# Performance work log

Measured on AMD Instinct MI355X. Metric: run time of the kernel, lower is better.

Reference implementation:

```python
import jax, jax.numpy as jnp
import numpy as np

UP = 4  # FCUUp up_stride
EPS_FCU = 1e-6
EPS_NL = 1e-5


def setup_inputs() -> dict:
    key = jax.random.key(0)
    ks = jax.random.split(key, 24)
    B, E, C, CI = 8, 768, 256, 128
    H, W = 14, 14
    x_t = jax.random.normal(ks[0], (B, 1 + H * W, E), jnp.float32)
    x_cnn = jax.random.normal(ks[1], (B, C, H * UP, W * UP), jnp.float32)
    s = 0.02
    return {
        'x_t': x_t,
        'x_cnn': x_cnn,
        # FCUUp: conv_project (E->C) + BN
        'Wp': jax.random.normal(ks[2], (C, E), jnp.float32) * s,
        'bp': jnp.zeros((C,), jnp.float32),
        'g1': jnp.ones((C,), jnp.float32),
        'b1': jnp.zeros((C,), jnp.float32),
        'rm1': jax.random.normal(ks[3], (C,), jnp.float32) * 0.1,
        'rv1': jax.random.uniform(ks[4], (C,), jnp.float32, 0.5, 1.5),
        # NLBlockND (embedded): g, theta, phi 1x1 convs C->CI
        'Wg': jax.random.normal(ks[5], (CI, C), jnp.float32) * s,
        'bg': jnp.zeros((CI,), jnp.float32),
        'Wth': jax.random.normal(ks[6], (CI, C), jnp.float32) * s,
        'bth': jnp.zeros((CI,), jnp.float32),
        'Wph': jax.random.normal(ks[7], (CI, C), jnp.float32) * s,
        'bph': jnp.zeros((CI,), jnp.float32),
        # W_z: 1x1 conv CI->C + BN
        'Wz': jax.random.normal(ks[8], (C, CI), jnp.float32) * s,
        'bz': jnp.zeros((C,), jnp.float32),
        'g2': jax.random.normal(ks[9], (C,), jnp.float32) * 0.1,
        'b2': jax.random.normal(ks[10], (C,), jnp.float32) * 0.1,
        'rm2': jax.random.normal(ks[11], (C,), jnp.float32) * 0.1,
        'rv2': jax.random.uniform(ks[12], (C,), jnp.float32, 0.5, 1.5),
    }


def _bn(x, gamma, beta, mean, var, eps):
    # eval-mode BatchNorm2d over channel axis 1 of BCHW
    inv = gamma / jnp.sqrt(var + eps)
    return x * inv[None, :, None, None] + (beta - mean * inv)[None, :, None, None]


def _conv1x1(x, w, b):
    # x: BCHW, w: [O, C] -> BOHW
    return jnp.einsum('oc,bchw->bohw', w, x) + b[None, :, None, None]


def reference(x_t, x_cnn, Wp, bp, g1, b1, rm1, rv1, Wg, bg, Wth, bth, Wph, bph, Wz, bz, g2, b2, rm2, rv2):
    B, Nc, H2, W2 = x_cnn.shape
    H, W = H2 // UP, W2 // UP
    CI = Wg.shape[0]
    # --- FCUUp: tokens -> feature map ---
    xr = x_t[:, 1:].transpose(0, 2, 1).reshape(B, -1, H, W)  # B,E,H,W
    xr = jax.nn.relu(_bn(_conv1x1(xr, Wp, bp), g1, b1, rm1, rv1, EPS_FCU))
    x_up = jnp.repeat(jnp.repeat(xr, UP, axis=2), UP, axis=3)  # nearest interp -> B,C,H2,W2
    # --- NLBlockND embedded: this=x_cnn, other=x_up ---
    N = H2 * W2
    g_x = _conv1x1(x_cnn, Wg, bg).reshape(B, CI, N).transpose(0, 2, 1)   # B,N,CI
    theta = _conv1x1(x_cnn, Wth, bth).reshape(B, CI, N)                  # B,CI,N
    phi = _conv1x1(x_up, Wph, bph).reshape(B, CI, N)                     # B,CI,N
    f = jnp.einsum('bim,bin->bmn', phi, theta)  # B,N,N
    f_div_C = jax.nn.softmax(f, axis=-1)
    y = jnp.einsum('bmn,bni->bmi', f_div_C, g_x)          # B,N,CI
    y = y.transpose(0, 2, 1).reshape(B, CI, H2, W2)
    W_y = _bn(_conv1x1(y, Wz, bz), g2, b2, rm2, rv2, EPS_NL)
    return W_y + x_cnn
```

## Files before the change

### kernel.cpp

```cpp
#include <hip/hip_runtime.h>
#include <hip/hip_bf16.h>

#define B_ 8
#define E_ 768
#define C_ 256
#define CI_ 128
#define NQ_ 196
#define N_ 3136

typedef short bf16x8 __attribute__((ext_vector_type(8)));
typedef float f32x4 __attribute__((ext_vector_type(4)));

__device__ __forceinline__ ushort f2bf(float x) {
    union { float f; uint u; } v; v.f = x;
    uint r = v.u + 0x7FFFu + ((v.u >> 16) & 1u);
    return (ushort)(r >> 16);
}
__device__ __forceinline__ uint pack2(float a, float b) {
    return (uint)f2bf(a) | ((uint)f2bf(b) << 16);
}

__global__ __launch_bounds__(256) void k0_prep(
    const float* __restrict__ x_cnn, ushort* __restrict__ xT,
    const float* __restrict__ Wth, const float* __restrict__ Wg,
    const float* __restrict__ Wp, const float* __restrict__ g1, const float* __restrict__ rv1,
    const float* __restrict__ Wph,
    ushort* __restrict__ Wcomb, ushort* __restrict__ Wp_bf, ushort* __restrict__ Wph_bf,
    float* __restrict__ y_ws, float* __restrict__ rowsum)
{
    __shared__ float Xs[64][68];
    int bx = blockIdx.x;
    int t = threadIdx.x;
    if (bx >= 1568) {
        int idx = (bx - 1568) * 256 + t;
        int o = idx >> 8, c = idx & 255;
        float v = (o < 128) ? Wth[o * 256 + c] : Wg[(o - 128) * 256 + c];
        Wcomb[idx] = f2bf(v);
        for (int i = idx; i < 196608; i += 65536) {
            int oo = i / 768;
            float inv1 = g1[oo] * rsqrtf(rv1[oo] + 1e-6f);
            Wp_bf[i] = f2bf(Wp[i] * inv1);
        }
        if (idx < 32768) Wph_bf[idx] = f2bf(Wph[idx]);
        if (idx < 2048) rowsum[idx] = 0.0f;
        for (int i = idx; i < B_ * NQ_ * CI_; i += 65536) y_ws[i] = 0.0f;
        return;
    }
    int b = bx & 7; int rest = bx >> 3;
    int ct = rest & 3, nt = rest >> 2;
    int c0 = ct * 64, n0 = nt * 64;
    #pragma unroll
    for (int rr = 0; rr < 4; ++rr) {
        int idx = t + rr * 256;
        int c = idx >> 4, n4 = idx & 15;
        float4 v = *(const float4*)(x_cnn + ((size_t)(b * C_) + c0 + c) * N_ + n0 + n4 * 4);
        *(float4*)(&Xs[c][n4 * 4]) = v;
    }
    __syncthreads();
    int n = t & 63, cc = t >> 6;
    ushort vals[16];
    #pragma unroll
    for (int j = 0; j < 16; ++j)
        vals[j] = f2bf(Xs[cc * 16 + j][n]);
    ushort* outp = xT + ((size_t)(b * N_) + n0 + n) * 256 + c0 + cc * 16;
    *(uint4*)(outp) = *(const uint4*)(&vals[0]);
    *(uint4*)(outp + 8) = *(const uint4*)(&vals[8]);
}

__global__ __launch_bounds__(256) void k1a_proj(
    const float* __restrict__ x_t, const ushort* __restrict__ Wp_bf,
    const float* __restrict__ bp, const float* __restrict__ g1, const float* __restrict__ b1,
    const float* __restrict__ rm1, const float* __restrict__ rv1,
    ushort* __restrict__ xact)
{
    __shared__ ushort Al[32 * 40];
    __shared__ ushort Bl[64 * 40];
    int bx = blockIdx.x;
    int b = bx & 7; int rest = bx >> 3;
    int mt = rest & 7, nt = rest >> 3;
    int q0 = mt * 32, c0 = nt * 64;
    int t = threadIdx.x;
    int lane = t & 63, w = t >> 6;

    int arow = t >> 3, ac4 = t & 7;
    bool arow_ok = (q0 + arow) < NQ_;
    const float* gax = x_t + (size_t)b * 197 * 768 + (size_t)(1 + q0 + arow) * 768 + ac4 * 4;
    int brow = t >> 2, bc = t & 3;
    const ushort* gb = Wp_bf + (size_t)(c0 + brow) * 768 + bc * 8;
    ushort* la = &Al[arow * 40 + ac4 * 4];
    ushort* lb = &Bl[brow * 40 + bc * 8];

    f32x4 acc[2];
    acc[0] = (f32x4){0.f, 0.f, 0.f, 0.f};
    acc[1] = (f32x4){0.f, 0.f, 0.f, 0.f};

    int am = (lane & 15) * 40 + (lane >> 4) * 8;
    int bn = (w * 16 + (lane & 15)) * 40 + (lane >> 4) * 8;

    uint2 aw; aw.x = 0; aw.y = 0;
    if (arow_ok) { float4 x0 = *(const float4*)(gax); aw.x = pack2(x0.x, x0.y); aw.y = pack2(x0.z, x0.w); }
    uint4 bw = *(const uint4*)(gb);

    for (int ks = 0; ks < 24; ++ks) {
        __syncthreads();
        *(uint2*)la = aw;
        *(uint4*)lb = bw;
        __syncthreads();
        if (ks + 1 < 24) {
            aw.x = 0; aw.y = 0;
            if (arow_ok) {
                float4 x0 = *(const float4*)(gax + (ks + 1) * 32);
                aw.x = pack2(x0.x, x0.y); aw.y = pack2(x0.z, x0.w);
            }
            bw = *(const uint4*)(gb + (ks + 1) * 32);
        }
        bf16x8 af0 = *(const bf16x8*)(&Al[am]);
        bf16x8 af1 = *(const bf16x8*)(&Al[am + 16 * 40]);
        bf16x8 bfv = *(const bf16x8*)(&Bl[bn]);
        acc[0] = __builtin_amdgcn_mfma_f32_16x16x32_bf16(af0, bfv, acc[0], 0, 0, 0);
        acc[1] = __builtin_amdgcn_mfma_f32_16x16x32_bf16(af1, bfv, acc[1], 0, 0, 0);
    }

    int r4 = (lane >> 4) * 4;
    int cn = lane & 15;
    int c = c0 + w * 16 + cn;
    float inv1 = g1[c] * rsqrtf(rv1[c] + 1e-6f);
    float badd = bp[c] * inv1 + b1[c] - rm1[c] * inv1;
    #pragma unroll
    for (int fm = 0; fm < 2; ++fm) {
        int q = q0 + fm * 16 + r4;
        #pragma unroll
        for (int r = 0; r < 4; ++r) {
            float vv = fmaxf(acc[fm][r] + badd, 0.0f);
            xact[((size_t)((b << 8) + q + r)) * 256 + c] = f2bf(vv);
        }
    }
}

__global__ __launch_bounds__(256) void k1b_phi(
    const ushort* __restrict__ xact, const ushort* __restrict__ Wph_bf,
    const float* __restrict__ bph, ushort* __restrict__ phi_bf)
{
    __shared__ ushort Al[64 * 40];
    __shared__ ushort Bl[64 * 40];
    int bx = blockIdx.x;
    int b = bx & 7; int rest = bx >> 3;
    int mt = rest & 3, nt = rest >> 2;
    int q0 = mt * 64, i0 = nt * 64;
    int t = threadIdx.x;
    int lane = t & 63, w = t >> 6;
    int wm = w >> 1, wn = w & 1;
    int row = t >> 2, chunk = t & 3;

    const ushort* ga = xact + ((size_t)((b << 8) + q0 + row)) * 256 + chunk * 8;
    const ushort* gb = Wph_bf + (size_t)(i0 + row) * 256 + chunk * 8;
    ushort* la = &Al[row * 40 + chunk * 8];
    ushort* lb = &Bl[row * 40 + chunk * 8];

    f32x4 acc[2][2];
    #pragma unroll
    for (int a = 0; a < 2; ++a)
        #pragma unroll
        for (int bb = 0; bb < 2; ++bb) acc[a][bb] = (f32x4){0.f, 0.f, 0.f, 0.f};

    int am = (wm * 32 + (lane & 15)) * 40 + (lane >> 4) * 8;
    int bn = (wn * 32 + (lane & 15)) * 40 + (lane >> 4) * 8;

    uint4 aw = *(const uint4*)(ga);
    uint4 bw = *(const uint4*)(gb);
    for (int ks = 0; ks < 8; ++ks) {
        __syncthreads();
        *(uint4*)la = aw;
        *(uint4*)lb = bw;
        __syncthreads();
        if (ks + 1 < 8) {
            aw = *(const uint4*)(ga + (ks + 1) * 32);
            bw = *(const uint4*)(gb + (ks + 1) * 32);
        }
        bf16x8 af[2], bfv[2];
        #pragma unroll
        for (int fm = 0; fm < 2; ++fm) af[fm] = *(const bf16x8*)(&Al[am + fm * 16 * 40]);
        #pragma unroll
        for (int fn = 0; fn < 2; ++fn) bfv[fn] = *(const bf16x8*)(&Bl[bn + fn * 16 * 40]);
        #pragma unroll
        for (int fm = 0; fm < 2; ++fm)
            #pragma unroll
            for (int fn = 0; fn < 2; ++fn)
                acc[fm][fn] = __builtin_amdgcn_mfma_f32_16x16x32_bf16(af[fm], bfv[fn], acc[fm][fn], 0, 0, 0);
    }

    int r4 = (lane >> 4) * 4;
    int cn = lane & 15;
    #pragma unroll
    for (int fn = 0; fn < 2; ++fn) {
        int i = i0 + wn * 32 + fn * 16 + cn;
        float bias = bph[i];
        #pragma unroll
        for (int fm = 0; fm < 2; ++fm) {
            int q = q0 + wm * 32 + fm * 16 + r4;
            #pragma unroll
            for (int r = 0; r < 4; ++r) {
                ushort val = ((q + r) < NQ_) ? f2bf(acc[fm][fn][r] + bias) : (ushort)0;
                phi_bf[((size_t)((b << 8) + q + r)) * 128 + i] = val;
            }
        }
    }
}

__global__ __launch_bounds__(256) void k2_mfma(
    const ushort* __restrict__ Wcomb, const float* __restrict__ bth, const float* __restrict__ bg,
    const ushort* __restrict__ xT, ushort* __restrict__ thT, ushort* __restrict__ gT)
{
    __shared__ ushort Al[128 * 40];
    __shared__ ushort Bl[64 * 40];
    int bx = blockIdx.x;
    int b = bx & 7; int rest = bx >> 3;
    int mt = rest & 1, nt = rest >> 1;
    int o0 = mt * 128, n0 = nt * 64;
    int t = threadIdx.x;
    int lane = t & 63, w = t >> 6;
    int wm = w >> 1, wn = w & 1;
    int cn = lane & 15, kc = lane >> 4;

    int arow = t >> 1, ach = t & 1;
    const ushort* ga = Wcomb + (size_t)(o0 + arow) * 256 + ach * 8;
    int brow = t >> 2, bch = t & 3;
    const ushort* gb = xT + ((size_t)(b * N_) + n0 + brow) * 256 + bch * 8;
    ushort* la = &Al[arow * 40 + ach * 8];
    ushort* lb = &Bl[brow * 40 + bch * 8];

    f32x4 acc[4][2];
    #pragma unroll
    for (int a = 0; a < 4; ++a)
        #pragma unroll
        for (int bb = 0; bb < 2; ++bb) acc[a][bb] = (f32x4){0.f, 0.f, 0.f, 0.f};

    int am = (wm * 64 + cn) * 40 + kc * 8;
    int bn = (wn * 32 + cn) * 40 + kc * 8;

    uint4 aw0 = *(const uint4*)(ga);
    uint4 aw1 = *(const uint4*)(ga + 16);
    uint4 bw = *(const uint4*)(gb);
    for (int ks = 0; ks < 8; ++ks) {
        __syncthreads();
        *(uint4*)la = aw0;
        *(uint4*)(la + 16) = aw1;
        *(uint4*)lb = bw;
        __syncthreads();
        if (ks + 1 < 8) {
            aw0 = *(const uint4*)(ga + (ks + 1) * 32);
            aw1 = *(const uint4*)(ga + (ks + 1) * 32 + 16);
            bw = *(const uint4*)(gb + (ks + 1) * 32);
        }
        bf16x8 af[4], bfv[2];
        #pragma unroll
        for (int fm = 0; fm < 4; ++fm) af[fm] = *(const bf16x8*)(&Al[am + fm * 16 * 40]);
        #pragma unroll
        for (int fn = 0; fn < 2; ++fn) bfv[fn] = *(const bf16x8*)(&Bl[bn + fn * 16 * 40]);
        #pragma unroll
        for (int fm = 0; fm < 4; ++fm)
            #pragma unroll
            for (int fn = 0; fn < 2; ++fn)
                acc[fm][fn] = __builtin_amdgcn_mfma_f32_16x16x32_bf16(af[fm], bfv[fn], acc[fm][fn], 0, 0, 0);
    }

    int r4 = kc * 4;
    if (mt == 0) {
        #pragma unroll
        for (int fm = 0; fm < 4; ++fm) {
            int ob = wm * 64 + fm * 16 + r4;
            #pragma unroll
            for (int fn = 0; fn < 2; ++fn) {
                int n = n0 + wn * 32 + fn * 16 + cn;
                ushort4 v;
                v.x = f2bf(acc[fm][fn][0] + bth[ob + 0]);
                v.y = f2bf(acc[fm][fn][1] + bth[ob + 1]);
                v.z = f2bf(acc[fm][fn][2] + bth[ob + 2]);
                v.w = f2bf(acc[fm][fn][3] + bth[ob + 3]);
                *(ushort4*)(&thT[((size_t)(b * N_) + n) * 128 + ob]) = v;
            }
        }
    } else {
        #pragma unroll
        for (int fm = 0; fm < 4; ++fm) {
            int og = wm * 64 + fm * 16 + r4;
            #pragma unroll
            for (int fn = 0; fn < 2; ++fn) {
                int n = n0 + wn * 32 + fn * 16 + cn;
                #pragma unroll
                for (int r = 0; r < 4; ++r)
                    gT[((size_t)(b * 128) + og + r) * N_ + n] = f2bf(acc[fm][fn][r] + bg[og + r]);
            }
        }
    }
}

__global__ __launch_bounds__(256, 2) void k3_flash(
    const ushort* __restrict__ phi_bf, const ushort* __restrict__ thT,
    const ushort* __restrict__ gT, float* __restrict__ y_ws, float* __restrict__ rowsum)
{
    __shared__ ushort Qs[32 * 136];
    __shared__ ushort Kt[64 * 136];
    __shared__ ushort Gt[128 * 72];
    __shared__ ushort Ps[32 * 72];
    int bx = blockIdx.x;
    int b = bx & 7; int rr_ = bx >> 3;
    int qt = rr_ % 7, ksp = rr_ / 7;
    int q0 = qt * 32;
    int nb0 = ksp * 448;
    int t = threadIdx.x;
    int lane = t & 63, w = t >> 6;
    int cn = lane & 15, kc = lane >> 4;

    #pragma unroll
    for (int rr = 0; rr < 2; ++rr) {
        int idx = t + rr * 256;
        int q = idx >> 4, ch = idx & 15;
        uint4 v = *(const uint4*)(phi_bf + ((size_t)((b << 8) + q0 + q)) * 128 + ch * 8);
        *(uint4*)(&Qs[q * 136 + ch * 8]) = v;
    }

    int krow = t >> 2, kch = t & 3;
    int grow = t >> 1, gch = t & 1;
    const ushort* gK = thT + ((size_t)(b * N_) + nb0 + krow) * 128 + kch * 8;
    const ushort* gG = gT + ((size_t)(b * 128) + grow) * N_ + nb0 + gch * 8;
    ushort* lK = &Kt[krow * 136 + kch * 8];
    ushort* lG = &Gt[grow * 72 + gch * 8];

    float rs[2][4] = {{0, 0, 0, 0}, {0, 0, 0, 0}};
    f32x4 yacc[2][2];
    #pragma unroll
    for (int a = 0; a < 2; ++a)
        #pragma unroll
        for (int bb = 0; bb < 2; ++bb) yacc[a][bb] = (f32x4){0.f, 0.f, 0.f, 0.f};

    for (int s = 0; s < 7; ++s) {
        __syncthreads();
        {
            uint4 kv[4], gv[4];
            #pragma unroll
            for (int it = 0; it < 4; ++it) {
                kv[it] = *(const uint4*)(gK + it * 32);
                gv[it] = *(const uint4*)(gG + it * 16);
            }
            #pragma unroll
            for (int it = 0; it < 4; ++it) {
                *(uint4*)(lK + it * 32) = kv[it];
                *(uint4*)(lG + it * 16) = gv[it];
            }
        }
        gK += (size_t)64 * 128;
        gG += 64;
        __syncthreads();
        f32x4 f0 = (f32x4){0.f, 0.f, 0.f, 0.f};
        f32x4 f1 = (f32x4){0.f, 0.f, 0.f, 0.f};
        #pragma unroll
        for (int k4 = 0; k4 < 4; ++k4) {
            bf16x8 af0 = *(const bf16x8*)(&Qs[cn * 136 + k4 * 32 + kc * 8]);
            bf16x8 af1 = *(const bf16x8*)(&Qs[(16 + cn) * 136 + k4 * 32 + kc * 8]);
            bf16x8 bk = *(const bf16x8*)(&Kt[(w * 16 + cn) * 136 + k4 * 32 + kc * 8]);
            f0 = __builtin_amdgcn_mfma_f32_16x16x32_bf16(af0, bk, f0, 0, 0, 0);
            f1 = __builtin_amdgcn_mfma_f32_16x16x32_bf16(af1, bk, f1, 0, 0, 0);
        }
        #pragma unroll
        for (int r2 = 0; r2 < 4; ++r2) {
            float e0 = __expf(f0[r2]);
            float e1 = __expf(f1[r2]);
            rs[0][r2] += e0; rs[1][r2] += e1;
            Ps[(kc * 4 + r2) * 72 + w * 16 + cn] = f2bf(e0);
            Ps[(16 + kc * 4 + r2) * 72 + w * 16 + cn] = f2bf(e1);
        }
        __syncthreads();
        #pragma unroll
        for (int k2 = 0; k2 < 2; ++k2) {
            bf16x8 pa0 = *(const bf16x8*)(&Ps[cn * 72 + k2 * 32 + kc * 8]);
            bf16x8 pa1 = *(const bf16x8*)(&Ps[(16 + cn) * 72 + k2 * 32 + kc * 8]);
            bf16x8 g0 = *(const bf16x8*)(&Gt[(w * 32 + cn) * 72 + k2 * 32 + kc * 8]);
            bf16x8 g1 = *(const bf16x8*)(&Gt[(w * 32 + 16 + cn) * 72 + k2 * 32 + kc * 8]);
            yacc[0][0] = __builtin_amdgcn_mfma_f32_16x16x32_bf16(pa0, g0, yacc[0][0], 0, 0, 0);
            yacc[0][1] = __builtin_amdgcn_mfma_f32_16x16x32_bf16(pa0, g1, yacc[0][1], 0, 0, 0);
            yacc[1][0] = __builtin_amdgcn_mfma_f32_16x16x32_bf16(pa1, g0, yacc[1][0], 0, 0, 0);
            yacc[1][1] = __builtin_amdgcn_mfma_f32_16x16x32_bf16(pa1, g1, yacc[1][1], 0, 0, 0);
        }
    }

    #pragma unroll
    for (int fm = 0; fm < 2; ++fm) {
        #pragma unroll
        for (int fn = 0; fn < 2; ++fn) {
            int i = w * 32 + fn * 16 + cn;
            #pragma unroll
            for (int r2 = 0; r2 < 4; ++r2) {
                int q = q0 + fm * 16 + kc * 4 + r2;
                if (q < NQ_)
                    atomicAdd(&y_ws[((size_t)(b * NQ_) + q) * 128 + i], yacc[fm][fn][r2]);
            }
        }
    }
    #pragma unroll
    for (int off = 1; off <= 8; off <<= 1) {
        #pragma unroll
        for (int fm = 0; fm < 2; ++fm)
            #pragma unroll
            for (int r2 = 0; r2 < 4; ++r2)
                rs[fm][r2] += __shfl_xor(rs[fm][r2], off);
    }
    if (cn == 0) {
        #pragma unroll
        for (int fm = 0; fm < 2; ++fm)
            #pragma unroll
            for (int r2 = 0; r2 < 4; ++r2)
                atomicAdd(&rowsum[(b << 8) + q0 + fm * 16 + kc * 4 + r2], rs[fm][r2]);
    }
}

__global__ __launch_bounds__(256) void k4a_z(
    const float* __restrict__ y_ws, const float* __restrict__ rowsum,
    const float* __restrict__ Wz, const float* __restrict__ bz,
    const float* __restrict__ g2, const float* __restrict__ b2,
    const float* __restrict__ rm2, const float* __restrict__ rv2,
    float* __restrict__ z_ws)
{
    __shared__ float ys[8][128];
    int bx = blockIdx.x;
    int b = bx / 25, qt = bx % 25;
    int q0 = qt * 8;
    int t = threadIdx.x;
    #pragma unroll
    for (int rr = 0; rr < 4; ++rr) {
        int idx = t + rr * 256;
        int p = idx >> 7, ii = idx & 127;
        int q = q0 + p;
        float v = 0.0f;
        if (q < NQ_) {
            float inv = 1.0f / rowsum[(b << 8) + q];
            v = y_ws[(size_t)b * NQ_ * CI_ + (size_t)q * CI_ + ii] * inv;
        }
        ys[p][ii] = v;
    }
    __syncthreads();
    int c = t;
    float acc[8] = {0, 0, 0, 0, 0, 0, 0, 0};
    const float* wrow = Wz + (size_t)c * 128;
    for (int i4 = 0; i4 < 32; ++i4) {
        float4 w = *(const float4*)(wrow + i4 * 4);
        #pragma unroll
        for (int p = 0; p < 8; ++p) {
            float4 yv = *(const float4*)(&ys[p][i4 * 4]);
            acc[p] += w.x * yv.x + w.y * yv.y + w.z * yv.z + w.w * yv.w;
        }
    }
    float inv2 = g2[c] * rsqrtf(rv2[c] + 1e-5f);
    float add2 = b2[c] - rm2[c] * inv2;
    float bzc = bz[c];
    #pragma unroll
    for (int p = 0; p < 8; ++p) {
        int q = q0 + p;
        if (q < NQ_)
            z_ws[(size_t)b * C_ * NQ_ + (size_t)c * NQ_ + q] = (acc[p] + bzc) * inv2 + add2;
    }
}

__global__ __launch_bounds__(256) void k4b_out(
    const float* __restrict__ x_cnn, const float* __restrict__ z_ws, float* __restrict__ out)
{
    int idx = blockIdx.x * 256 + threadIdx.x;
    int w4 = idx % 14;
    int rest = idx / 14;
    int h = rest % 56;
    rest /= 56;
    int c = rest % 256;
    int b = rest / 256;
    int q = (h >> 2) * 14 + w4;
    float z = z_ws[((size_t)b * C_ + c) * NQ_ + q];
    float4 xv = *(const float4*)(x_cnn + (size_t)idx * 4);
    float4 o = make_float4(xv.x + z, xv.y + z, xv.z + z, xv.w + z);
    *(float4*)(out + (size_t)idx * 4) = o;
}

extern "C" void kernel_launch(void* const* d_in, const int* in_sizes, int n_in,
                              void* d_out, int out_size, void* d_ws, size_t ws_size,
                              hipStream_t stream) {
    const float* x_t   = (const float*)d_in[0];
    const float* x_cnn = (const float*)d_in[1];
    const float* Wp  = (const float*)d_in[2];
    const float* bp  = (const float*)d_in[3];
    const float* g1  = (const float*)d_in[4];
    const float* b1  = (const float*)d_in[5];
    const float* rm1 = (const float*)d_in[6];
    const float* rv1 = (const float*)d_in[7];
    const float* Wg  = (const float*)d_in[8];
    const float* bg  = (const float*)d_in[9];
    const float* Wth = (const float*)d_in[10];
    const float* bth = (const float*)d_in[11];
    const float* Wph = (const float*)d_in[12];
    const float* bph = (const float*)d_in[13];
    const float* Wz  = (const float*)d_in[14];
    const float* bz  = (const float*)d_in[15];
    const float* g2  = (const float*)d_in[16];
    const float* b2  = (const float*)d_in[17];
    const float* rm2 = (const float*)d_in[18];
    const float* rv2 = (const float*)d_in[19];
    float* out = (float*)d_out;

    char* ws = (char*)d_ws;
    ushort* xT   = (ushort*)(ws);
    ushort* thT  = (ushort*)(ws + 12845056);
    ushort* gT   = (ushort*)(ws + 19267584);
    ushort* phi  = (ushort*)(ws + 25690112);
    float*  y_ws = (float*)(ws + 26214400);
    float*  z_ws = (float*)(ws + 27017216);
    ushort* Wcomb= (ushort*)(ws + 28622848);
    ushort* Wp_bf= (ushort*)(ws + 28753920);
    ushort* Wph_bf=(ushort*)(ws + 29147136);
    ushort* xact = (ushort*)(ws + 29212672);
    float*  rowsum=(float*)(ws + 30261248);

    k0_prep<<<dim3(1824), dim3(256), 0, stream>>>(x_cnn, xT, Wth, Wg, Wp, g1, rv1, Wph,
                                                  Wcomb, Wp_bf, Wph_bf, y_ws, rowsum);
    k1a_proj<<<dim3(256), dim3(256), 0, stream>>>(x_t, Wp_bf, bp, g1, b1, rm1, rv1, xact);
    k1b_phi<<<dim3(64), dim3(256), 0, stream>>>(xact, Wph_bf, bph, phi);
    k2_mfma<<<dim3(784), dim3(256), 0, stream>>>(Wcomb, bth, bg, xT, thT, gT);
    k3_flash<<<dim3(392), dim3(256), 0, stream>>>(phi, thT, gT, y_ws, rowsum);
    k4a_z<<<dim3(200), dim3(256), 0, stream>>>(y_ws, rowsum, Wz, bz, g2, b2, rm2, rv2, z_ws);
    k4b_out<<<dim3(6272), dim3(256), 0, stream>>>(x_cnn, z_ws, out);
}
```

Before: 86.51 us.

## Load MFMA operands directly from global memory instead of staging through LDS

The phi, theta/g projection and flash-attention kernels now read MFMA operand fragments straight from global memory (relying on L1/L2 caching) rather than cooperatively staging tiles into shared memory. This removes the LDS writes and most __syncthreads barriers, and frees LDS so more blocks can be resident. The attention kernel keeps only the Q and P tiles in LDS, pads P rows to 76, and drops the launch-bounds occupancy hint. In exchange, each wave issues uncoalesced 16-byte loads with redundant traffic across waves, which may be limited by cache bandwidth and latency.

```diff
diff --git a/kernel.cpp b/kernel.cpp
--- a/kernel.cpp
+++ b/kernel.cpp
@@ -141,8 +141,6 @@
     const ushort* __restrict__ xact, const ushort* __restrict__ Wph_bf,
     const float* __restrict__ bph, ushort* __restrict__ phi_bf)
 {
-    __shared__ ushort Al[64 * 40];
-    __shared__ ushort Bl[64 * 40];
     int bx = blockIdx.x;
     int b = bx & 7; int rest = bx >> 3;
     int mt = rest & 3, nt = rest >> 2;
@@ -150,12 +148,7 @@
     int t = threadIdx.x;
     int lane = t & 63, w = t >> 6;
     int wm = w >> 1, wn = w & 1;
-    int row = t >> 2, chunk = t & 3;
-
-    const ushort* ga = xact + ((size_t)((b << 8) + q0 + row)) * 256 + chunk * 8;
-    const ushort* gb = Wph_bf + (size_t)(i0 + row) * 256 + chunk * 8;
-    ushort* la = &Al[row * 40 + chunk * 8];
-    ushort* lb = &Bl[row * 40 + chunk * 8];
+    int cn = lane & 15, kc = lane >> 4;
 
     f32x4 acc[2][2];
     #pragma unroll
@@ -163,25 +156,16 @@
         #pragma unroll
         for (int bb = 0; bb < 2; ++bb) acc[a][bb] = (f32x4){0.f, 0.f, 0.f, 0.f};
 
-    int am = (wm * 32 + (lane & 15)) * 40 + (lane >> 4) * 8;
-    int bn = (wn * 32 + (lane & 15)) * 40 + (lane >> 4) * 8;
-
-    uint4 aw = *(const uint4*)(ga);
-    uint4 bw = *(const uint4*)(gb);
+    const ushort* ga = xact + ((size_t)((b << 8) + q0 + wm * 32 + cn)) * 256 + kc * 8;
+    const ushort* gb = Wph_bf + (size_t)(i0 + wn * 32 + cn) * 256 + kc * 8;
+
+    #pragma unroll 2
     for (int ks = 0; ks < 8; ++ks) {
-        __syncthreads();
-        *(uint4*)la = aw;
-        *(uint4*)lb = bw;
-        __syncthreads();
-        if (ks + 1 < 8) {
-            aw = *(const uint4*)(ga + (ks + 1) * 32);
-            bw = *(const uint4*)(gb + (ks + 1) * 32);
-        }
         bf16x8 af[2], bfv[2];
         #pragma unroll
-        for (int fm = 0; fm < 2; ++fm) af[fm] = *(const bf16x8*)(&Al[am + fm * 16 * 40]);
-        #pragma unroll
-        for (int fn = 0; fn < 2; ++fn) bfv[fn] = *(const bf16x8*)(&Bl[bn + fn * 16 * 40]);
+        for (int fm = 0; fm < 2; ++fm) af[fm] = *(const bf16x8*)(ga + fm * 16 * 256 + ks * 32);
+        #pragma unroll
+        for (int fn = 0; fn < 2; ++fn) bfv[fn] = *(const bf16x8*)(gb + fn * 16 * 256 + ks * 32);
         #pragma unroll
         for (int fm = 0; fm < 2; ++fm)
             #pragma unroll
@@ -189,8 +173,7 @@
                 acc[fm][fn] = __builtin_amdgcn_mfma_f32_16x16x32_bf16(af[fm], bfv[fn], acc[fm][fn], 0, 0, 0);
     }
 
-    int r4 = (lane >> 4) * 4;
-    int cn = lane & 15;
+    int r4 = kc * 4;
     #pragma unroll
     for (int fn = 0; fn < 2; ++fn) {
         int i = i0 + wn * 32 + fn * 16 + cn;
@@ -211,8 +194,6 @@
     const ushort* __restrict__ Wcomb, const float* __restrict__ bth, const float* __restrict__ bg,
     const ushort* __restrict__ xT, ushort* __restrict__ thT, ushort* __restrict__ gT)
 {
-    __shared__ ushort Al[128 * 40];
-    __shared__ ushort Bl[64 * 40];
     int bx = blockIdx.x;
     int b = bx & 7; int rest = bx >> 3;
     int mt = rest & 1, nt = rest >> 1;
@@ -222,41 +203,22 @@
     int wm = w >> 1, wn = w & 1;
     int cn = lane & 15, kc = lane >> 4;
 
-    int arow = t >> 1, ach = t & 1;
-    const ushort* ga = Wcomb + (size_t)(o0 + arow) * 256 + ach * 8;
-    int brow = t >> 2, bch = t & 3;
-    const ushort* gb = xT + ((size_t)(b * N_) + n0 + brow) * 256 + bch * 8;
-    ushort* la = &Al[arow * 40 + ach * 8];
-    ushort* lb = &Bl[brow * 40 + bch * 8];
-
     f32x4 acc[4][2];
     #pragma unroll
     for (int a = 0; a < 4; ++a)
         #pragma unroll
         for (int bb = 0; bb < 2; ++bb) acc[a][bb] = (f32x4){0.f, 0.f, 0.f, 0.f};
 
-    int am = (wm * 64 + cn) * 40 + kc * 8;
-    int bn = (wn * 32 + cn) * 40 + kc * 8;
-
-    uint4 aw0 = *(const uint4*)(ga);
-    uint4 aw1 = *(const uint4*)(ga + 16);
-    uint4 bw = *(const uint4*)(gb);
+    const ushort* ga = Wcomb + (size_t)(o0 + wm * 64 + cn) * 256 + kc * 8;
+    const ushort* gb = xT + ((size_t)(b * N_) + n0 + wn * 32 + cn) * 256 + kc * 8;
+
+    #pragma unroll 2
     for (int ks = 0; ks < 8; ++ks) {
-        __syncthreads();
-        *(uint4*)la = aw0;
-        *(uint4*)(la + 16) = aw1;
-        *(uint4*)lb = bw;
-        __syncthreads();
-        if (ks + 1 < 8) {
-            aw0 = *(const uint4*)(ga + (ks + 1) * 32);
-            aw1 = *(const uint4*)(ga + (ks + 1) * 32 + 16);
-            bw = *(const uint4*)(gb + (ks + 1) * 32);
-        }
         bf16x8 af[4], bfv[2];
         #pragma unroll
-        for (int fm = 0; fm < 4; ++fm) af[fm] = *(const bf16x8*)(&Al[am + fm * 16 * 40]);
-        #pragma unroll
-        for (int fn = 0; fn < 2; ++fn) bfv[fn] = *(const bf16x8*)(&Bl[bn + fn * 16 * 40]);
+        for (int fm = 0; fm < 4; ++fm) af[fm] = *(const bf16x8*)(ga + fm * 16 * 256 + ks * 32);
+        #pragma unroll
+        for (int fn = 0; fn < 2; ++fn) bfv[fn] = *(const bf16x8*)(gb + fn * 16 * 256 + ks * 32);
         #pragma unroll
         for (int fm = 0; fm < 4; ++fm)
             #pragma unroll
@@ -295,14 +257,12 @@
     }
 }
 
-__global__ __launch_bounds__(256, 2) void k3_flash(
+__global__ __launch_bounds__(256) void k3_flash(
     const ushort* __restrict__ phi_bf, const ushort* __restrict__ thT,
     const ushort* __restrict__ gT, float* __restrict__ y_ws, float* __restrict__ rowsum)
 {
     __shared__ ushort Qs[32 * 136];
-    __shared__ ushort Kt[64 * 136];
-    __shared__ ushort Gt[128 * 72];
-    __shared__ ushort Ps[32 * 72];
+    __shared__ ushort Ps[32 * 76];
     int bx = blockIdx.x;
     int b = bx & 7; int rr_ = bx >> 3;
     int qt = rr_ % 7, ksp = rr_ / 7;
@@ -319,13 +279,10 @@
         uint4 v = *(const uint4*)(phi_bf + ((size_t)((b << 8) + q0 + q)) * 128 + ch * 8);
         *(uint4*)(&Qs[q * 136 + ch * 8]) = v;
     }
-
-    int krow = t >> 2, kch = t & 3;
-    int grow = t >> 1, gch = t & 1;
-    const ushort* gK = thT + ((size_t)(b * N_) + nb0 + krow) * 128 + kch * 8;
-    const ushort* gG = gT + ((size_t)(b * 128) + grow) * N_ + nb0 + gch * 8;
-    ushort* lK = &Kt[krow * 136 + kch * 8];
-    ushort* lG = &Gt[grow * 72 + gch * 8];
+    __syncthreads();
+
+    const ushort* thb = thT + (size_t)(b * N_) * 128;
+    const ushort* gbb = gT + (size_t)(b * 128) * N_;
 
     float rs[2][4] = {{0, 0, 0, 0}, {0, 0, 0, 0}};
     f32x4 yacc[2][2];
@@ -335,30 +292,14 @@
         for (int bb = 0; bb < 2; ++bb) yacc[a][bb] = (f32x4){0.f, 0.f, 0.f, 0.f};
 
     for (int s = 0; s < 7; ++s) {
-        __syncthreads();
-        {
-            uint4 kv[4], gv[4];
-            #pragma unroll
-            for (int it = 0; it < 4; ++it) {
-                kv[it] = *(const uint4*)(gK + it * 32);
-                gv[it] = *(const uint4*)(gG + it * 16);
-            }
-            #pragma unroll
-            for (int it = 0; it < 4; ++it) {
-                *(uint4*)(lK + it * 32) = kv[it];
-                *(uint4*)(lG + it * 16) = gv[it];
-            }
-        }
-        gK += (size_t)64 * 128;
-        gG += 64;
-        __syncthreads();
+        int ns = nb0 + s * 64;
         f32x4 f0 = (f32x4){0.f, 0.f, 0.f, 0.f};
         f32x4 f1 = (f32x4){0.f, 0.f, 0.f, 0.f};
         #pragma unroll
         for (int k4 = 0; k4 < 4; ++k4) {
+            bf16x8 bk = *(const bf16x8*)(thb + (size_t)(ns + w * 16 + cn) * 128 + k4 * 32 + kc * 8);
             bf16x8 af0 = *(const bf16x8*)(&Qs[cn * 136 + k4 * 32 + kc * 8]);
             bf16x8 af1 = *(const bf16x8*)(&Qs[(16 + cn) * 136 + k4 * 32 + kc * 8]);
-            bf16x8 bk = *(const bf16x8*)(&Kt[(w * 16 + cn) * 136 + k4 * 32 + kc * 8]);
             f0 = __builtin_amdgcn_mfma_f32_16x16x32_bf16(af0, bk, f0, 0, 0, 0);
             f1 = __builtin_amdgcn_mfma_f32_16x16x32_bf16(af1, bk, f1, 0, 0, 0);
         }
@@ -367,21 +308,22 @@
             float e0 = __expf(f0[r2]);
             float e1 = __expf(f1[r2]);
             rs[0][r2] += e0; rs[1][r2] += e1;
-            Ps[(kc * 4 + r2) * 72 + w * 16 + cn] = f2bf(e0);
-            Ps[(16 + kc * 4 + r2) * 72 + w * 16 + cn] = f2bf(e1);
+            Ps[(kc * 4 + r2) * 76 + w * 16 + cn] = f2bf(e0);
+            Ps[(16 + kc * 4 + r2) * 76 + w * 16 + cn] = f2bf(e1);
         }
         __syncthreads();
         #pragma unroll
         for (int k2 = 0; k2 < 2; ++k2) {
-            bf16x8 pa0 = *(const bf16x8*)(&Ps[cn * 72 + k2 * 32 + kc * 8]);
-            bf16x8 pa1 = *(const bf16x8*)(&Ps[(16 + cn) * 72 + k2 * 32 + kc * 8]);
-            bf16x8 g0 = *(const bf16x8*)(&Gt[(w * 32 + cn) * 72 + k2 * 32 + kc * 8]);
-            bf16x8 g1 = *(const bf16x8*)(&Gt[(w * 32 + 16 + cn) * 72 + k2 * 32 + kc * 8]);
+            bf16x8 pa0 = *(const bf16x8*)(&Ps[cn * 76 + k2 * 32 + kc * 8]);
+            bf16x8 pa1 = *(const bf16x8*)(&Ps[(16 + cn) * 76 + k2 * 32 + kc * 8]);
+            bf16x8 g0 = *(const bf16x8*)(gbb + (size_t)(w * 32 + cn) * N_ + ns + k2 * 32 + kc * 8);
+            bf16x8 g1 = *(const bf16x8*)(gbb + (size_t)(w * 32 + 16 + cn) * N_ + ns + k2 * 32 + kc * 8);
             yacc[0][0] = __builtin_amdgcn_mfma_f32_16x16x32_bf16(pa0, g0, yacc[0][0], 0, 0, 0);
             yacc[0][1] = __builtin_amdgcn_mfma_f32_16x16x32_bf16(pa0, g1, yacc[0][1], 0, 0, 0);
             yacc[1][0] = __builtin_amdgcn_mfma_f32_16x16x32_bf16(pa1, g0, yacc[1][0], 0, 0, 0);
             yacc[1][1] = __builtin_amdgcn_mfma_f32_16x16x32_bf16(pa1, g1, yacc[1][1], 0, 0, 0);
         }
+        __syncthreads();
     }
 
     #pragma unroll
```

After: 106.0 us. 1.22x slower.

## Merge launches: fold projection into prep, phi into theta/g, z-GEMM into output

Applied to the files above, without the earlier changes.

Cuts the pipeline from seven launches to four. The token projection now runs as extra blocks of the prep kernel and folds the BN scale into Wp on the fly, so the separate Wp_bf conversion pass is gone. The phi GEMM runs as extra blocks of the theta/g GEMM kernel. The W_z conv now uses bf16 MFMA and is fused with the residual add and nearest upsampling, so z_ws is never stored or reloaded. The trade-offs are a fused output kernel with only 112 blocks, which may underuse the GPU on a bandwidth-bound write, and bf16 precision for the W_z GEMM.

```diff
diff --git a/kernel.cpp b/kernel.cpp
--- a/kernel.cpp
+++ b/kernel.cpp
@@ -20,28 +20,96 @@
     return (uint)f2bf(a) | ((uint)f2bf(b) << 16);
 }
 
-__global__ __launch_bounds__(256) void k0_prep(
+__global__ __launch_bounds__(256) void k01(
     const float* __restrict__ x_cnn, ushort* __restrict__ xT,
     const float* __restrict__ Wth, const float* __restrict__ Wg,
-    const float* __restrict__ Wp, const float* __restrict__ g1, const float* __restrict__ rv1,
-    const float* __restrict__ Wph,
-    ushort* __restrict__ Wcomb, ushort* __restrict__ Wp_bf, ushort* __restrict__ Wph_bf,
-    float* __restrict__ y_ws, float* __restrict__ rowsum)
+    const float* __restrict__ Wph, const float* __restrict__ Wz,
+    const float* __restrict__ x_t, const float* __restrict__ Wp,
+    const float* __restrict__ bp, const float* __restrict__ g1, const float* __restrict__ b1,
+    const float* __restrict__ rm1, const float* __restrict__ rv1,
+    ushort* __restrict__ Wcomb, ushort* __restrict__ Wph_bf, ushort* __restrict__ Wz_bf,
+    float* __restrict__ y_ws, float* __restrict__ rowsum, ushort* __restrict__ xact)
 {
     __shared__ float Xs[64][68];
+    __shared__ ushort Al[32 * 40];
+    __shared__ ushort Bl[64 * 40];
     int bx = blockIdx.x;
     int t = threadIdx.x;
+
+    if (bx >= 1824) {
+        int bx2 = bx - 1824;
+        int b = bx2 & 7; int rest = bx2 >> 3;
+        int mt = rest & 7, nt = rest >> 3;
+        int q0 = mt * 32, c0 = nt * 64;
+        int lane = t & 63, w = t >> 6;
+
+        int arow = t >> 3, ac4 = t & 7;
+        bool arow_ok = (q0 + arow) < NQ_;
+        const float* gax = x_t + (size_t)b * 197 * 768 + (size_t)(1 + q0 + arow) * 768 + ac4 * 4;
+        int brow = t >> 2, bc = t & 3;
+        const float* gbf = Wp + (size_t)(c0 + brow) * 768 + bc * 8;
+        float binv = g1[c0 + brow] * rsqrtf(rv1[c0 + brow] + 1e-6f);
+        ushort* la = &Al[arow * 40 + ac4 * 4];
+        ushort* lb = &Bl[brow * 40 + bc * 8];
+
+        f32x4 acc0 = (f32x4){0.f, 0.f, 0.f, 0.f};
+        f32x4 acc1 = (f32x4){0.f, 0.f, 0.f, 0.f};
+        int am = (lane & 15) * 40 + (lane >> 4) * 8;
+        int bn = (w * 16 + (lane & 15)) * 40 + (lane >> 4) * 8;
+
+        uint2 aw; aw.x = 0; aw.y = 0;
+        if (arow_ok) { float4 x0 = *(const float4*)(gax); aw.x = pack2(x0.x, x0.y); aw.y = pack2(x0.z, x0.w); }
+        uint4 bw;
+        {
+            float4 u = *(const float4*)(gbf), v = *(const float4*)(gbf + 4);
+            bw.x = pack2(u.x * binv, u.y * binv); bw.y = pack2(u.z * binv, u.w * binv);
+            bw.z = pack2(v.x * binv, v.y * binv); bw.w = pack2(v.z * binv, v.w * binv);
+        }
+
+        for (int ks = 0; ks < 24; ++ks) {
+            __syncthreads();
+            *(uint2*)la = aw;
+            *(uint4*)lb = bw;
+            __syncthreads();
+            if (ks + 1 < 24) {
+                aw.x = 0; aw.y = 0;
+                if (arow_ok) {
+                    float4 x0 = *(const float4*)(gax + (ks + 1) * 32);
+                    aw.x = pack2(x0.x, x0.y); aw.y = pack2(x0.z, x0.w);
+                }
+                float4 u = *(const float4*)(gbf + (ks + 1) * 32);
+                float4 v = *(const float4*)(gbf + (ks + 1) * 32 + 4);
+                bw.x = pack2(u.x * binv, u.y * binv); bw.y = pack2(u.z * binv, u.w * binv);
+                bw.z = pack2(v.x * binv, v.y * binv); bw.w = pack2(v.z * binv, v.w * binv);
+            }
+            bf16x8 af0 = *(const bf16x8*)(&Al[am]);
+            bf16x8 af1 = *(const bf16x8*)(&Al[am + 16 * 40]);
+            bf16x8 bfv = *(const bf16x8*)(&Bl[bn]);
+            acc0 = __builtin_amdgcn_mfma_f32_16x16x32_bf16(af0, bfv, acc0, 0, 0, 0);
+            acc1 = __builtin_amdgcn_mfma_f32_16x16x32_bf16(af1, bfv, acc1, 0, 0, 0);
+        }
+
+        int r4 = (lane >> 4) * 4;
+        int cn = lane & 15;
+        int c = c0 + w * 16 + cn;
+        float inv1 = g1[c] * rsqrtf(rv1[c] + 1e-6f);
+        float badd = bp[c] * inv1 + b1[c] - rm1[c] * inv1;
+        #pragma unroll
+        for (int r = 0; r < 4; ++r) {
+            float v0 = fmaxf(acc0[r] + badd, 0.0f);
+            float v1 = fmaxf(acc1[r] + badd, 0.0f);
+            xact[((size_t)((b << 8) + q0 + r4 + r)) * 256 + c] = f2bf(v0);
+            xact[((size_t)((b << 8) + q0 + 16 + r4 + r)) * 256 + c] = f2bf(v1);
+        }
+        return;
+    }
     if (bx >= 1568) {
         int idx = (bx - 1568) * 256 + t;
         int o = idx >> 8, c = idx & 255;
         float v = (o < 128) ? Wth[o * 256 + c] : Wg[(o - 128) * 256 + c];
         Wcomb[idx] = f2bf(v);
-        for (int i = idx; i < 196608; i += 65536) {
-            int oo = i / 768;
-            float inv1 = g1[oo] * rsqrtf(rv1[oo] + 1e-6f);
-            Wp_bf[i] = f2bf(Wp[i] * inv1);
-        }
         if (idx < 32768) Wph_bf[idx] = f2bf(Wph[idx]);
+        if (idx < 32768) Wz_bf[idx] = f2bf(Wz[idx]);
         if (idx < 2048) rowsum[idx] = 0.0f;
         for (int i = idx; i < B_ * NQ_ * CI_; i += 65536) y_ws[i] = 0.0f;
         return;
@@ -67,158 +135,85 @@
     *(uint4*)(outp + 8) = *(const uint4*)(&vals[8]);
 }
 
-__global__ __launch_bounds__(256) void k1a_proj(
-    const float* __restrict__ x_t, const ushort* __restrict__ Wp_bf,
-    const float* __restrict__ bp, const float* __restrict__ g1, const float* __restrict__ b1,
-    const float* __restrict__ rm1, const float* __restrict__ rv1,
-    ushort* __restrict__ xact)
-{
-    __shared__ ushort Al[32 * 40];
-    __shared__ ushort Bl[64 * 40];
-    int bx = blockIdx.x;
-    int b = bx & 7; int rest = bx >> 3;
-    int mt = rest & 7, nt = rest >> 3;
-    int q0 = mt * 32, c0 = nt * 64;
-    int t = threadIdx.x;
-    int lane = t & 63, w = t >> 6;
-
-    int arow = t >> 3, ac4 = t & 7;
-    bool arow_ok = (q0 + arow) < NQ_;
-    const float* gax = x_t + (size_t)b * 197 * 768 + (size_t)(1 + q0 + arow) * 768 + ac4 * 4;
-    int brow = t >> 2, bc = t & 3;
-    const ushort* gb = Wp_bf + (size_t)(c0 + brow) * 768 + bc * 8;
-    ushort* la = &Al[arow * 40 + ac4 * 4];
-    ushort* lb = &Bl[brow * 40 + bc * 8];
-
-    f32x4 acc[2];
-    acc[0] = (f32x4){0.f, 0.f, 0.f, 0.f};
-    acc[1] = (f32x4){0.f, 0.f, 0.f, 0.f};
-
-    int am = (lane & 15) * 40 + (lane >> 4) * 8;
-    int bn = (w * 16 + (lane & 15)) * 40 + (lane >> 4) * 8;
-
-    uint2 aw; aw.x = 0; aw.y = 0;
-    if (arow_ok) { float4 x0 = *(const float4*)(gax); aw.x = pack2(x0.x, x0.y); aw.y = pack2(x0.z, x0.w); }
-    uint4 bw = *(const uint4*)(gb);
-
-    for (int ks = 0; ks < 24; ++ks) {
-        __syncthreads();
-        *(uint2*)la = aw;
-        *(uint4*)lb = bw;
-        __syncthreads();
-        if (ks + 1 < 24) {
-            aw.x = 0; aw.y = 0;
-            if (arow_ok) {
-                float4 x0 = *(const float4*)(gax + (ks + 1) * 32);
-                aw.x = pack2(x0.x, x0.y); aw.y = pack2(x0.z, x0.w);
-            }
-            bw = *(const uint4*)(gb + (ks + 1) * 32);
-        }
-        bf16x8 af0 = *(const bf16x8*)(&Al[am]);
-        bf16x8 af1 = *(const bf16x8*)(&Al[am + 16 * 40]);
-        bf16x8 bfv = *(const bf16x8*)(&Bl[bn]);
-        acc[0] = __builtin_amdgcn_mfma_f32_16x16x32_bf16(af0, bfv, acc[0], 0, 0, 0);
-        acc[1] = __builtin_amdgcn_mfma_f32_16x16x32_bf16(af1, bfv, acc[1], 0, 0, 0);
-    }
-
-    int r4 = (lane >> 4) * 4;
-    int cn = lane & 15;
-    int c = c0 + w * 16 + cn;
-    float inv1 = g1[c] * rsqrtf(rv1[c] + 1e-6f);
-    float badd = bp[c] * inv1 + b1[c] - rm1[c] * inv1;
-    #pragma unroll
-    for (int fm = 0; fm < 2; ++fm) {
-        int q = q0 + fm * 16 + r4;
-        #pragma unroll
-        for (int r = 0; r < 4; ++r) {
-            float vv = fmaxf(acc[fm][r] + badd, 0.0f);
-            xact[((size_t)((b << 8) + q + r)) * 256 + c] = f2bf(vv);
-        }
-    }
-}
-
-__global__ __launch_bounds__(256) void k1b_phi(
+__global__ __launch_bounds__(256) void k12(
+    const ushort* __restrict__ Wcomb, const float* __restrict__ bth, const float* __restrict__ bg,
+    const ushort* __restrict__ xT, ushort* __restrict__ thT, ushort* __restrict__ gT,
     const ushort* __restrict__ xact, const ushort* __restrict__ Wph_bf,
     const float* __restrict__ bph, ushort* __restrict__ phi_bf)
 {
-    __shared__ ushort Al[64 * 40];
+    __shared__ ushort Al[128 * 40];
     __shared__ ushort Bl[64 * 40];
-    int bx = blockIdx.x;
-    int b = bx & 7; int rest = bx >> 3;
-    int mt = rest & 3, nt = rest >> 2;
-    int q0 = mt * 64, i0 = nt * 64;
     int t = threadIdx.x;
     int lane = t & 63, w = t >> 6;
-    int wm = w >> 1, wn = w & 1;
-    int row = t >> 2, chunk = t & 3;
-
-    const ushort* ga = xact + ((size_t)((b << 8) + q0 + row)) * 256 + chunk * 8;
-    const ushort* gb = Wph_bf + (size_t)(i0 + row) * 256 + chunk * 8;
-    ushort* la = &Al[row * 40 + chunk * 8];
-    ushort* lb = &Bl[row * 40 + chunk * 8];
-
-    f32x4 acc[2][2];
-    #pragma unroll
-    for (int a = 0; a < 2; ++a)
-        #pragma unroll
-        for (int bb = 0; bb < 2; ++bb) acc[a][bb] = (f32x4){0.f, 0.f, 0.f, 0.f};
-
-    int am = (wm * 32 + (lane & 15)) * 40 + (lane >> 4) * 8;
-    int bn = (wn * 32 + (lane & 15)) * 40 + (lane >> 4) * 8;
-
-    uint4 aw = *(const uint4*)(ga);
-    uint4 bw = *(const uint4*)(gb);
-    for (int ks = 0; ks < 8; ++ks) {
-        __syncthreads();
-        *(uint4*)la = aw;
-        *(uint4*)lb = bw;
-        __syncthreads();
-        if (ks + 1 < 8) {
-            aw = *(const uint4*)(ga + (ks + 1) * 32);
-            bw = *(const uint4*)(gb + (ks + 1) * 32);
-        }
-        bf16x8 af[2], bfv[2];
-        #pragma unroll
-        for (int fm = 0; fm < 2; ++fm) af[fm] = *(const bf16x8*)(&Al[am + fm * 16 * 40]);
-        #pragma unroll
-        for (int fn = 0; fn < 2; ++fn) bfv[fn] = *(const bf16x8*)(&Bl[bn + fn * 16 * 40]);
-        #pragma unroll
-        for (int fm = 0; fm < 2; ++fm)
-            #pragma unroll
-            for (int fn = 0; fn < 2; ++fn)
-                acc[fm][fn] = __builtin_amdgcn_mfma_f32_16x16x32_bf16(af[fm], bfv[fn], acc[fm][fn], 0, 0, 0);
-    }
-
-    int r4 = (lane >> 4) * 4;
-    int cn = lane & 15;
-    #pragma unroll
-    for (int fn = 0; fn < 2; ++fn) {
-        int i = i0 + wn * 32 + fn * 16 + cn;
-        float bias = bph[i];
-        #pragma unroll
-        for (int fm = 0; fm < 2; ++fm) {
-            int q = q0 + wm * 32 + fm * 16 + r4;
-            #pragma unroll
-            for (int r = 0; r < 4; ++r) {
-                ushort val = ((q + r) < NQ_) ? f2bf(acc[fm][fn][r] + bias) : (ushort)0;
-                phi_bf[((size_t)((b << 8) + q + r)) * 128 + i] = val;
-            }
-        }
-    }
-}
-
-__global__ __launch_bounds__(256) void k2_mfma(
-    const ushort* __restrict__ Wcomb, const float* __restrict__ bth, const float* __restrict__ bg,
-    const ushort* __restrict__ xT, ushort* __restrict__ thT, ushort* __restrict__ gT)
-{
-    __shared__ ushort Al[128 * 40];
-    __shared__ ushort Bl[64 * 40];
+
+    if (blockIdx.x >= 784) {
+        int bx2 = blockIdx.x - 784;
+        int b = bx2 & 7; int rest = bx2 >> 3;
+        int mt = rest & 3, nt = rest >> 2;
+        int q0 = mt * 64, i0 = nt * 64;
+        int wm = w >> 1, wn = w & 1;
+        int row = t >> 2, chunk = t & 3;
+
+        const ushort* ga = xact + ((size_t)((b << 8) + q0 + row)) * 256 + chunk * 8;
+        const ushort* gb = Wph_bf + (size_t)(i0 + row) * 256 + chunk * 8;
+        ushort* la = &Al[row * 40 + chunk * 8];
+        ushort* lb = &Bl[row * 40 + chunk * 8];
+
+        f32x4 acc[2][2];
+        #pragma unroll
+        for (int a = 0; a < 2; ++a)
+            #pragma unroll
+            for (int bb = 0; bb < 2; ++bb) acc[a][bb] = (f32x4){0.f, 0.f, 0.f, 0.f};
+
+        int am = (wm * 32 + (lane & 15)) * 40 + (lane >> 4) * 8;
+        int bn = (wn * 32 + (lane & 15)) * 40 + (lane >> 4) * 8;
+
+        uint4 aw = *(const uint4*)(ga);
+        uint4 bw = *(const uint4*)(gb);
+        for (int ks = 0; ks < 8; ++ks) {
+            __syncthreads();
+            *(uint4*)la = aw;
+            *(uint4*)lb = bw;
+            __syncthreads();
+            if (ks + 1 < 8) {
+                aw = *(const uint4*)(ga + (ks + 1) * 32);
+                bw = *(const uint4*)(gb + (ks + 1) * 32);
+            }
+            bf16x8 af[2], bfv[2];
+            #pragma unroll
+            for (int fm = 0; fm < 2; ++fm) af[fm] = *(const bf16x8*)(&Al[am + fm * 16 * 40]);
+            #pragma unroll
+            for (int fn = 0; fn < 2; ++fn) bfv[fn] = *(const bf16x8*)(&Bl[bn + fn * 16 * 40]);
+            #pragma unroll
+            for (int fm = 0; fm < 2; ++fm)
+                #pragma unroll
+                for (int fn = 0; fn < 2; ++fn)
+                    acc[fm][fn] = __builtin_amdgcn_mfma_f32_16x16x32_bf16(af[fm], bfv[fn], acc[fm][fn], 0, 0, 0);
+        }
+
+        int r4 = (lane >> 4) * 4;
+        int cn = lane & 15;
+        #pragma unroll
+        for (int fn = 0; fn < 2; ++fn) {
+            int i = i0 + wn * 32 + fn * 16 + cn;
+            float bias = bph[i];
+            #pragma unroll
+            for (int fm = 0; fm < 2; ++fm) {
+                int q = q0 + wm * 32 + fm * 16 + r4;
+                #pragma unroll
+                for (int r = 0; r < 4; ++r) {
+                    ushort val = ((q + r) < NQ_) ? f2bf(acc[fm][fn][r] + bias) : (ushort)0;
+                    phi_bf[((size_t)((b << 8) + q + r)) * 128 + i] = val;
+                }
+            }
+        }
+        return;
+    }
+
     int bx = blockIdx.x;
     int b = bx & 7; int rest = bx >> 3;
     int mt = rest & 1, nt = rest >> 1;
     int o0 = mt * 128, n0 = nt * 64;
-    int t = threadIdx.x;
-    int lane = t & 63, w = t >> 6;
     int wm = w >> 1, wn = w & 1;
     int cn = lane & 15, kc = lane >> 4;
 
@@ -414,68 +409,89 @@
     }
 }
 
-__global__ __launch_bounds__(256) void k4a_z(
+__global__ __launch_bounds__(256) void k45(
     const float* __restrict__ y_ws, const float* __restrict__ rowsum,
-    const float* __restrict__ Wz, const float* __restrict__ bz,
-    const float* __restrict__ g2, const float* __restrict__ b2,
+    const ushort* __restrict__ Wz_bf,
+    const float* __restrict__ bz, const float* __restrict__ g2, const float* __restrict__ b2,
     const float* __restrict__ rm2, const float* __restrict__ rv2,
-    float* __restrict__ z_ws)
+    const float* __restrict__ x_cnn, float* __restrict__ out)
 {
-    __shared__ float ys[8][128];
+    __shared__ ushort Al[16 * 136];
+    __shared__ ushort Bl[256 * 40];
+    __shared__ float zs[16 * 260];
     int bx = blockIdx.x;
-    int b = bx / 25, qt = bx % 25;
-    int q0 = qt * 8;
+    int b = bx & 7, hq = bx >> 3;
+    int q0 = hq * 14;
     int t = threadIdx.x;
-    #pragma unroll
-    for (int rr = 0; rr < 4; ++rr) {
-        int idx = t + rr * 256;
-        int p = idx >> 7, ii = idx & 127;
-        int q = q0 + p;
-        float v = 0.0f;
-        if (q < NQ_) {
-            float inv = 1.0f / rowsum[(b << 8) + q];
-            v = y_ws[(size_t)b * NQ_ * CI_ + (size_t)q * CI_ + ii] * inv;
-        }
-        ys[p][ii] = v;
+    int lane = t & 63, w = t >> 6;
+    int cn = lane & 15, kc = lane >> 4;
+
+    {
+        int row = t >> 4, i0 = (t & 15) * 8;
+        uint4 aw = make_uint4(0, 0, 0, 0);
+        if (row < 14) {
+            float inv = 1.0f / rowsum[(b << 8) + q0 + row];
+            const float* yp = y_ws + ((size_t)(b * NQ_) + q0 + row) * 128 + i0;
+            float4 u = *(const float4*)(yp), v = *(const float4*)(yp + 4);
+            aw.x = pack2(u.x * inv, u.y * inv); aw.y = pack2(u.z * inv, u.w * inv);
+            aw.z = pack2(v.x * inv, v.y * inv); aw.w = pack2(v.z * inv, v.w * inv);
+        }
+        *(uint4*)(&Al[row * 136 + i0]) = aw;
+    }
+
+    f32x4 acc[4];
+    #pragma unroll
+    for (int a = 0; a < 4; ++a) acc[a] = (f32x4){0.f, 0.f, 0.f, 0.f};
+    int am = cn * 136 + kc * 8;
+    int bn = (w * 64 + cn) * 40 + kc * 8;
+
+    #pragma unroll
+    for (int ks = 0; ks < 4; ++ks) {
+        __syncthreads();
+        {
+            const ushort* wp = Wz_bf + (size_t)t * 128 + ks * 32;
+            uint4 b0 = *(const uint4*)(wp);
+            uint4 b1v = *(const uint4*)(wp + 8);
+            *(uint4*)(&Bl[t * 40]) = b0;
+            *(uint4*)(&Bl[t * 40 + 8]) = b1v;
+        }
+        __syncthreads();
+        bf16x8 af = *(const bf16x8*)(&Al[am + ks * 32]);
+        #pragma unroll
+        for (int fc = 0; fc < 4; ++fc) {
+            bf16x8 bv = *(const bf16x8*)(&Bl[bn + fc * 16 * 40]);
+            acc[fc] = __builtin_amdgcn_mfma_f32_16x16x32_bf16(af, bv, acc[fc], 0, 0, 0);
+        }
+    }
+
+    #pragma unroll
+    for (int fc = 0; fc < 4; ++fc) {
+        int c = w * 64 + fc * 16 + cn;
+        float inv2 = g2[c] * rsqrtf(rv2[c] + 1e-5f);
+        float add2 = b2[c] - rm2[c] * inv2;
+        float bzc = bz[c];
+        #pragma unroll
+        for (int r = 0; r < 4; ++r) {
+            int q = kc * 4 + r;
+            zs[q * 260 + c] = (acc[fc][r] + bzc) * inv2 + add2;
+        }
     }
     __syncthreads();
-    int c = t;
-    float acc[8] = {0, 0, 0, 0, 0, 0, 0, 0};
-    const float* wrow = Wz + (size_t)c * 128;
-    for (int i4 = 0; i4 < 32; ++i4) {
-        float4 w = *(const float4*)(wrow + i4 * 4);
-        #pragma unroll
-        for (int p = 0; p < 8; ++p) {
-            float4 yv = *(const float4*)(&ys[p][i4 * 4]);
-            acc[p] += w.x * yv.x + w.y * yv.y + w.z * yv.z + w.w * yv.w;
-        }
-    }
-    float inv2 = g2[c] * rsqrtf(rv2[c] + 1e-5f);
-    float add2 = b2[c] - rm2[c] * inv2;
-    float bzc = bz[c];
-    #pragma unroll
-    for (int p = 0; p < 8; ++p) {
-        int q = q0 + p;
-        if (q < NQ_)
-            z_ws[(size_t)b * C_ * NQ_ + (size_t)c * NQ_ + q] = (acc[p] + bzc) * inv2 + add2;
-    }
-}
-
-__global__ __launch_bounds__(256) void k4b_out(
-    const float* __restrict__ x_cnn, const float* __restrict__ z_ws, float* __restrict__ out)
-{
-    int idx = blockIdx.x * 256 + threadIdx.x;
-    int w4 = idx % 14;
-    int rest = idx / 14;
-    int h = rest % 56;
-    rest /= 56;
-    int c = rest % 256;
-    int b = rest / 256;
-    int q = (h >> 2) * 14 + w4;
-    float z = z_ws[((size_t)b * C_ + c) * NQ_ + q];
-    float4 xv = *(const float4*)(x_cnn + (size_t)idx * 4);
-    float4 o = make_float4(xv.x + z, xv.y + z, xv.z + z, xv.w + z);
-    *(float4*)(out + (size_t)idx * 4) = o;
+
+    if (t < 224) {
+        int c4 = t / 14, w4 = t % 14;
+        #pragma unroll
+        for (int ccg = 0; ccg < 16; ++ccg) {
+            int c = c4 * 16 + ccg;
+            float z = zs[w4 * 260 + c];
+            #pragma unroll
+            for (int dh = 0; dh < 4; ++dh) {
+                size_t off = ((size_t)(b * C_ + c)) * N_ + (size_t)(hq * 4 + dh) * 56 + w4 * 4;
+                float4 xv = *(const float4*)(x_cnn + off);
+                *(float4*)(out + off) = make_float4(xv.x + z, xv.y + z, xv.z + z, xv.w + z);
+            }
+        }
+    }
 }
 
 extern "C" void kernel_launch(void* const* d_in, const int* in_sizes, int n_in,
@@ -504,24 +520,23 @@
     float* out = (float*)d_out;
 
     char* ws = (char*)d_ws;
-    ushort* xT   = (ushort*)(ws);
-    ushort* thT  = (ushort*)(ws + 12845056);
-    ushort* gT   = (ushort*)(ws + 19267584);
-    ushort* phi  = (ushort*)(ws + 25690112);
-    float*  y_ws = (float*)(ws + 26214400);
-    float*  z_ws = (float*)(ws + 27017216);
-    ushort* Wcomb= (ushort*)(ws + 28622848);
-    ushort* Wp_bf= (ushort*)(ws + 28753920);
-    ushort* Wph_bf=(ushort*)(ws + 29147136);
-    ushort* xact = (ushort*)(ws + 29212672);
-    float*  rowsum=(float*)(ws + 30261248);
-
-    k0_prep<<<dim3(1824), dim3(256), 0, stream>>>(x_cnn, xT, Wth, Wg, Wp, g1, rv1, Wph,
-                                                  Wcomb, Wp_bf, Wph_bf, y_ws, rowsum);
-    k1a_proj<<<dim3(256), dim3(256), 0, stream>>>(x_t, Wp_bf, bp, g1, b1, rm1, rv1, xact);
-    k1b_phi<<<dim3(64), dim3(256), 0, stream>>>(xact, Wph_bf, bph, phi);
-    k2_mfma<<<dim3(784), dim3(256), 0, stream>>>(Wcomb, bth, bg, xT, thT, gT);
+    ushort* xT    = (ushort*)(ws);
+    ushort* thT   = (ushort*)(ws + 12845056);
+    ushort* gT    = (ushort*)(ws + 19267584);
+    ushort* phi   = (ushort*)(ws + 25690112);
+    float*  y_ws  = (float*)(ws + 26214400);
+    ushort* Wcomb = (ushort*)(ws + 27017216);
+    ushort* Wph_bf= (ushort*)(ws + 27148288);
+    ushort* Wz_bf = (ushort*)(ws + 27213824);
+    ushort* xact  = (ushort*)(ws + 27279360);
+    float*  rowsum= (float*)(ws + 28327936);
+
+    k01<<<dim3(2080), dim3(256), 0, stream>>>(x_cnn, xT, Wth, Wg, Wph, Wz, x_t, Wp,
+                                              bp, g1, b1, rm1, rv1,
+                                              Wcomb, Wph_bf, Wz_bf, y_ws, rowsum, xact);
+    k12<<<dim3(848), dim3(256), 0, stream>>>(Wcomb, bth, bg, xT, thT, gT,
+                                             xact, Wph_bf, bph, phi);
     k3_flash<<<dim3(392), dim3(256), 0, stream>>>(phi, thT, gT, y_ws, rowsum);
-    k4a_z<<<dim3(200), dim3(256), 0, stream>>>(y_ws, rowsum, Wz, bz, g2, b2, rm2, rv2, z_ws);
-    k4b_out<<<dim3(6272), dim3(256), 0, stream>>>(x_cnn, z_ws, out);
-}
+    k45<<<dim3(112), dim3(256), 0, stream>>>(y_ws, rowsum, Wz_bf, bz, g2, b2, rm2, rv2,
+                                             x_cnn, out);
+}
```

New measurement: 71.38 us. 1.21x faster.
